# Kernel optimization log

Hardware: AMD Instinct MI355X
Metric: run time of the kernel (lower is better)

## Reference

```python
import jax, jax.numpy as jnp
import numpy as np

HID = 1024
NH = 16
HD = HID // NH  # 64


def _lin_params(key, fan_in, fan_out):
    k1, k2 = jax.random.split(key)
    lim = 1.0 / np.sqrt(fan_in)
    W = jax.random.uniform(k1, (fan_in, fan_out), jnp.float32, -lim, lim)
    b = jax.random.uniform(k2, (fan_out,), jnp.float32, -lim, lim)
    return W, b


def setup_inputs() -> dict:
    key = jax.random.key(0)
    ks = jax.random.split(key, 12)
    B, S = 4, 1024
    inp = {
        'query': jax.random.normal(ks[0], (B, S, HID), jnp.float32),
        'key': jax.random.normal(ks[1], (B, S, HID), jnp.float32),
        'value': jax.random.normal(ks[2], (B, S, HID), jnp.float32),
    }
    inp['Wq'], inp['bq'] = _lin_params(ks[3], HID, HID)
    inp['Wk'], inp['bk'] = _lin_params(ks[4], HID, HID)
    inp['Wv'], inp['bv'] = _lin_params(ks[5], HID, HID)
    inp['Wp'], inp['bp'] = _lin_params(ks[6], HID, HID)
    inp['Wup'], inp['bup'] = _lin_params(ks[7], HD, 1)
    inp['Wud'], inp['bud'] = _lin_params(ks[8], HD, 1)
    inp['Wus'], inp['bus'] = _lin_params(ks[9], HID, NH)
    inp['Wo'], inp['bo'] = _lin_params(ks[10], HID, HID)
    return inp


def _split_heads(x, B, S):
    # [B,S,HID] -> [B,NH,S,HD]
    return x.reshape(B, S, NH, HD).transpose(0, 2, 1, 3)


def reference(query, key, value, Wq, bq, Wk, bk, Wv, bv, Wp, bp,
              Wup, bup, Wud, bud, Wus, bus, Wo, bo):
    B, S, _ = query.shape
    len_q = S

    q = query @ Wq + bq   # [B,S,HID]
    k = key @ Wk + bk
    v = value @ Wv + bv

    # Gaussian-window positional bias (per head, per query position)
    p = _split_heads(q @ Wp + bp, B, S)              # [B,NH,S,HD]
    tp = jnp.tanh(p)
    p_i = tp @ Wup + bup                             # [B,NH,S,1]
    z_i = tp @ Wud + bud                             # [B,NH,S,1]
    cen_pos = len_q * jax.nn.sigmoid(p_i)            # [B,NH,S,1]
    win_size = len_q * jax.nn.sigmoid(z_i)           # [B,NH,S,1]
    pos = jnp.arange(len_q, dtype=q.dtype)[None, None, None, :]  # [1,1,1,S]
    bias = (pos - cen_pos) ** 2 / (0.5 * win_size ** 2)          # [B,NH,S,S]

    # per-head alpha gate from raw query
    alpha = jax.nn.sigmoid(query @ Wus + bus)        # [B,S,NH]
    alpha = alpha.reshape(B, S, NH, 1).transpose(0, 2, 1, 3)  # [B,NH,S,1]

    qh = _split_heads(q, B, S)
    kh = _split_heads(k, B, S)
    vh = _split_heads(v, B, S)

    scale = 1.0 / jnp.sqrt(jnp.asarray(HD, q.dtype))
    scores = jnp.einsum('bhqd,bhkd->bhqk', qh, kh) * scale
    scores = scores - alpha * bias                   # inject gated Gaussian bias
    attn = jax.nn.softmax(scores, axis=-1)           # [B,NH,S,S]

    out = jnp.einsum('bhqk,bhkd->bhqd', attn, vh)    # [B,NH,S,HD]
    x = out.transpose(0, 2, 1, 3).reshape(B, S, HID)
    x = x @ Wo + bo
    return x, attn
```

## Files before the change

kernel.cpp:

```cpp
#include <hip/hip_runtime.h>
#include <hip/hip_bf16.h>
#include <math.h>

#define S_LEN 1024
#define HIDN  1024
#define NHEAD 16
#define HDIM  64
#define BATCH 4
#define MTOT  (BATCH * S_LEN)

typedef __attribute__((ext_vector_type(8))) short          bf16v8;
typedef __attribute__((ext_vector_type(8))) unsigned short u16v8;
typedef __attribute__((ext_vector_type(4))) unsigned short u16v4;
typedef __attribute__((ext_vector_type(4))) float          f32v4;

__device__ __forceinline__ unsigned short f2bf_rne(float x) {
    unsigned int u = __float_as_uint(x);
    unsigned int r = (u + 0x7fffu + ((u >> 16) & 1u)) >> 16;
    return (unsigned short)r;
}
__device__ __forceinline__ float bf2f(unsigned short h) {
    return __uint_as_float(((unsigned int)h) << 16);
}
__device__ __forceinline__ void split2(float x, unsigned short& h, unsigned short& l) {
    h = f2bf_rne(x);
    l = f2bf_rne(x - bf2f(h));
}

__global__ __launch_bounds__(256) void split_w4(
    const float* __restrict__ W0, const float* __restrict__ W1,
    const float* __restrict__ W2, const float* __restrict__ W3,
    unsigned short* __restrict__ Hbase, unsigned short* __restrict__ Lbase)
{
    __shared__ float T[64][65];
    const int t  = threadIdx.x;
    const int k0 = blockIdx.y * 64;
    const int n0 = blockIdx.x * 64;
    const int z  = blockIdx.z;
    const float* W = (z == 0) ? W0 : (z == 1) ? W1 : (z == 2) ? W2 : W3;
    unsigned short* H = Hbase + (size_t)z * 1024 * 1024;
    unsigned short* L = Lbase + (size_t)z * 1024 * 1024;

    const int r = t >> 4;
    const int c = (t & 15) * 4;
#pragma unroll
    for (int i = 0; i < 4; ++i) {
        const int rr = r + i * 16;
        const float4 v = *(const float4*)&W[(size_t)(k0 + rr) * 1024 + n0 + c];
        T[rr][c + 0] = v.x; T[rr][c + 1] = v.y;
        T[rr][c + 2] = v.z; T[rr][c + 3] = v.w;
    }
    __syncthreads();

    const int n  = t >> 2;
    const int ko = (t & 3) * 16;
    u16v8 h0, h1, l0, l1;
#pragma unroll
    for (int kk = 0; kk < 8; ++kk) {
        unsigned short hh, ll;
        split2(T[ko + kk][n], hh, ll);
        h0[kk] = hh; l0[kk] = ll;
    }
#pragma unroll
    for (int kk = 0; kk < 8; ++kk) {
        unsigned short hh, ll;
        split2(T[ko + 8 + kk][n], hh, ll);
        h1[kk] = hh; l1[kk] = ll;
    }
    unsigned short* Hp = &H[(size_t)(n0 + n) * 1024 + k0 + ko];
    unsigned short* Lp = &L[(size_t)(n0 + n) * 1024 + k0 + ko];
    *(u16v8*)(Hp)     = h0;
    *(u16v8*)(Hp + 8) = h1;
    *(u16v8*)(Lp)     = l0;
    *(u16v8*)(Lp + 8) = l1;
}

template<int AF32, int EPI>
__global__ __launch_bounds__(512, 2) void gemm_t(
    const float* __restrict__ Af,
    const unsigned short* __restrict__ Ah, const unsigned short* __restrict__ Al,
    const unsigned short* __restrict__ Bh, const unsigned short* __restrict__ Bl,
    const float* __restrict__ bias, float* __restrict__ Cf,
    unsigned short* __restrict__ Ch, unsigned short* __restrict__ Cl,
    const float* __restrict__ Wup, const float* __restrict__ Wud,
    const float* __restrict__ bup, const float* __restrict__ bud,
    const float* __restrict__ alpha, float* __restrict__ cenp,
    float* __restrict__ c0p)
{
    __shared__ short Ash[128][40];
    __shared__ short Asl[128][40];
    __shared__ short Bsh[64][40];
    __shared__ short Bsl[64][40];
    __shared__ float PSUP[2][128], PSUD[2][128];

    const int t    = threadIdx.x;
    const int bm   = blockIdx.y * 128;
    const int bn   = blockIdx.x * 64;
    const int lane = t & 63;
    const int wid  = t >> 6;
    const int wr   = wid >> 1;
    const int wc   = wid & 1;
    const int fr   = lane & 15;
    const int fq   = lane >> 4;
    const int ks   = fq * 8;

    f32v4 zero = {0.f, 0.f, 0.f, 0.f};
    f32v4 acc[2][2];
#pragma unroll
    for (int i = 0; i < 2; ++i)
#pragma unroll
        for (int j = 0; j < 2; ++j) acc[i][j] = zero;

    const int sra = t >> 2;
    const int sca = (t & 3) * 8;
    const int tb  = t & 255;
    const int srb = tb >> 2;
    const int scb = (tb & 3) * 8;
    const bool isBl = (t >= 256);
    const unsigned short* pB = isBl ? &Bl[(size_t)(bn + srb) * 1024 + scb]
                                    : &Bh[(size_t)(bn + srb) * 1024 + scb];
    const float* pAf = AF32 ? &Af[(size_t)(bm + sra) * 1024 + sca] : nullptr;
    const unsigned short* pAh = AF32 ? nullptr : &Ah[(size_t)(bm + sra) * 1024 + sca];
    const unsigned short* pAl = AF32 ? nullptr : &Al[(size_t)(bm + sra) * 1024 + sca];

    u16v8 rah, ral, rb;
    auto LOAD = [&](int k0) {
        if (AF32) {
            const float4 a0 = *(const float4*)(pAf + k0);
            const float4 a1 = *(const float4*)(pAf + k0 + 4);
            const float xs[8] = {a0.x, a0.y, a0.z, a0.w, a1.x, a1.y, a1.z, a1.w};
#pragma unroll
            for (int e = 0; e < 8; ++e) {
                unsigned short hh, ll;
                split2(xs[e], hh, ll);
                rah[e] = hh; ral[e] = ll;
            }
        } else {
            rah = *(const u16v8*)(pAh + k0);
            ral = *(const u16v8*)(pAl + k0);
        }
        rb = *(const u16v8*)(pB + k0);
    };

    LOAD(0);
    for (int k0 = 0; k0 < 1024; k0 += 32) {
        __syncthreads();
        *(u16v8*)&Ash[sra][sca] = rah;
        *(u16v8*)&Asl[sra][sca] = ral;
        if (isBl) *(u16v8*)&Bsl[srb][scb] = rb;
        else      *(u16v8*)&Bsh[srb][scb] = rb;
        __syncthreads();

        if (k0 + 32 < 1024) LOAD(k0 + 32);

        bf16v8 fah[2], fal[2], fbh[2], fbl[2];
#pragma unroll
        for (int i = 0; i < 2; ++i) {
            fah[i] = *(const bf16v8*)&Ash[wr * 32 + i * 16 + fr][ks];
            fal[i] = *(const bf16v8*)&Asl[wr * 32 + i * 16 + fr][ks];
        }
#pragma unroll
        for (int j = 0; j < 2; ++j) {
            fbh[j] = *(const bf16v8*)&Bsh[wc * 32 + j * 16 + fr][ks];
            fbl[j] = *(const bf16v8*)&Bsl[wc * 32 + j * 16 + fr][ks];
        }
#pragma unroll
        for (int i = 0; i < 2; ++i)
#pragma unroll
            for (int j = 0; j < 2; ++j) {
                acc[i][j] = __builtin_amdgcn_mfma_f32_16x16x32_bf16(
                    fah[i], fbh[j], acc[i][j], 0, 0, 0);
                acc[i][j] = __builtin_amdgcn_mfma_f32_16x16x32_bf16(
                    fah[i], fbl[j], acc[i][j], 0, 0, 0);
                acc[i][j] = __builtin_amdgcn_mfma_f32_16x16x32_bf16(
                    fal[i], fbh[j], acc[i][j], 0, 0, 0);
            }
    }

    if (EPI == 3) {
        float wupj[2], wudj[2];
        float bb[2];
#pragma unroll
        for (int j = 0; j < 2; ++j) {
            const int colL = wc * 32 + j * 16 + fr;
            wupj[j] = Wup[colL];
            wudj[j] = Wud[colL];
            bb[j]   = bias[bn + colL];
        }
        float su[2][4], sd[2][4];
#pragma unroll
        for (int i = 0; i < 2; ++i)
#pragma unroll
            for (int r = 0; r < 4; ++r) { su[i][r] = 0.f; sd[i][r] = 0.f; }
#pragma unroll
        for (int j = 0; j < 2; ++j)
#pragma unroll
            for (int i = 0; i < 2; ++i)
#pragma unroll
                for (int r = 0; r < 4; ++r) {
                    const float tv = tanhf(acc[i][j][r] + bb[j]);
                    su[i][r] = fmaf(tv, wupj[j], su[i][r]);
                    sd[i][r] = fmaf(tv, wudj[j], sd[i][r]);
                }
#pragma unroll
        for (int i = 0; i < 2; ++i)
#pragma unroll
            for (int r = 0; r < 4; ++r) {
                float a = su[i][r], d = sd[i][r];
                a += __shfl_xor(a, 1); d += __shfl_xor(d, 1);
                a += __shfl_xor(a, 2); d += __shfl_xor(d, 2);
                a += __shfl_xor(a, 4); d += __shfl_xor(d, 4);
                a += __shfl_xor(a, 8); d += __shfl_xor(d, 8);
                if (fr == 0) {
                    const int row = wr * 32 + i * 16 + fq * 4 + r;
                    PSUP[wc][row] = a;
                    PSUD[wc][row] = d;
                }
            }
        __syncthreads();
        if (t < 128) {
            const float ap = PSUP[0][t] + PSUP[1][t] + bup[0];
            const float az = PSUD[0][t] + PSUD[1][t] + bud[0];
            const float cenv = 1024.f / (1.f + expf(-ap));
            const float win  = 1024.f / (1.f + expf(-az));
            const int grow = bm + t;
            const int hd   = bn >> 6;
            const int zz   = (grow >> 10) * 16 + hd;
            const int s    = grow & 1023;
            const float al = alpha[(size_t)grow * 16 + hd];
            cenp[(size_t)zz * 1024 + s] = cenv;
            c0p[(size_t)zz * 1024 + s]  = al * 2.f / (win * win);
        }
        return;
    }

#pragma unroll
    for (int j = 0; j < 2; ++j) {
        const int col = bn + wc * 32 + j * 16 + fr;
        const float bb = bias[col];
#pragma unroll
        for (int i = 0; i < 2; ++i) {
            const int row0 = bm + wr * 32 + i * 16 + fq * 4;
            const f32v4 cv = acc[i][j];
            if (EPI == 2) {
                u16v4 h4, l4;
#pragma unroll
                for (int r = 0; r < 4; ++r) {
                    unsigned short hh, ll;
                    split2(cv[r] + bb, hh, ll);
                    h4[r] = hh; l4[r] = ll;
                }
                const size_t base =
                    ((size_t)((row0 >> 10) * 16 + (col >> 6)) * 64 + (col & 63)) * 1024
                    + (row0 & 1023);
                *(u16v4*)&Ch[base] = h4;
                *(u16v4*)&Cl[base] = l4;
            } else if (EPI == 1) {
#pragma unroll
                for (int r = 0; r < 4; ++r) {
                    unsigned short hh, ll;
                    split2(cv[r] + bb, hh, ll);
                    const size_t idx = (size_t)(row0 + r) * 1024 + col;
                    Ch[idx] = hh; Cl[idx] = ll;
                }
            } else {
#pragma unroll
                for (int r = 0; r < 4; ++r)
                    Cf[(size_t)(row0 + r) * 1024 + col] = cv[r] + bb;
            }
        }
    }
}

__global__ __launch_bounds__(256) void alpha_kernel(
    const float* __restrict__ X, const float* __restrict__ Wus,
    const float* __restrict__ bus, float* __restrict__ alpha)
{
    __shared__ float Ws[1024 * 16];
    const int t = threadIdx.x;
#pragma unroll
    for (int i = 0; i < 16; ++i) {
        const int idx = t + i * 256;
        *reinterpret_cast<float4*>(&Ws[idx * 4]) =
            *reinterpret_cast<const float4*>(&Wus[idx * 4]);
    }
    __syncthreads();

    const int r = t >> 4, c = t & 15;
    const size_t row = (size_t)blockIdx.x * 16 + r;
    const float* x = &X[row * 1024];
    float acc = 0.f;
    for (int kk = 0; kk < 1024; kk += 4) {
        const float4 xv = *reinterpret_cast<const float4*>(&x[kk]);
        acc = fmaf(xv.x, Ws[(kk + 0) * 16 + c], acc);
        acc = fmaf(xv.y, Ws[(kk + 1) * 16 + c], acc);
        acc = fmaf(xv.z, Ws[(kk + 2) * 16 + c], acc);
        acc = fmaf(xv.w, Ws[(kk + 3) * 16 + c], acc);
    }
    acc += bus[c];
    alpha[row * 16 + c] = 1.f / (1.f + expf(-acc));
}

#define M0_SHIFT 8.0f
__global__ __launch_bounds__(512, 2) void attn_fused(
    const unsigned short* __restrict__ qh, const unsigned short* __restrict__ ql,
    const unsigned short* __restrict__ kh, const unsigned short* __restrict__ kl,
    const unsigned short* __restrict__ vTh, const unsigned short* __restrict__ vTl,
    const float* __restrict__ cen, const float* __restrict__ c0,
    float* __restrict__ attn,
    unsigned short* __restrict__ oh, unsigned short* __restrict__ ol)
{
    __shared__ unsigned short KH[64][64], KL[64][64];
    __shared__ unsigned short VH[64][64], VL[64][64];
    __shared__ unsigned short PH[128][64], PL[128][64];
    __shared__ float CEN[128], C0S[128];
    __shared__ float LSUM[2][128];
    __shared__ float RINV[128];

    const int bid   = blockIdx.x;
    const int z     = ((bid >> 6) << 3) | (bid & 7);
    const int itile = (bid >> 3) & 7;
    const int i0    = itile * 128;
    const int bq    = z >> 4;
    const int hd    = z & 15;

    const int t    = threadIdx.x;
    const int lane = t & 63;
    const int wid  = t >> 6;
    const int wrp  = wid >> 1;
    const int wc   = wid & 1;
    const int fr   = lane & 15, fq = lane >> 4;

    if (t < 128) {
        CEN[t] = cen[(size_t)z * 1024 + i0 + t];
        C0S[t] = c0[(size_t)z * 1024 + i0 + t];
    }

    bf16v8 qfh_[2][2], qfl_[2][2];
#pragma unroll
    for (int i = 0; i < 2; ++i)
#pragma unroll
        for (int kk = 0; kk < 2; ++kk) {
            const size_t qa = (size_t)(bq * 1024 + i0 + wrp * 32 + i * 16 + fr) * 1024
                              + hd * 64 + kk * 32 + fq * 8;
            qfh_[i][kk] = *(const bf16v8*)&qh[qa];
            qfl_[i][kk] = *(const bf16v8*)&ql[qa];
        }

    float lsum[2][4];
#pragma unroll
    for (int i = 0; i < 2; ++i)
#pragma unroll
        for (int r = 0; r < 4; ++r) lsum[i][r] = 0.f;

    const f32v4 zero = {0.f, 0.f, 0.f, 0.f};

    const int srow = t >> 3;
    const int sseg = t & 7;
    const int ssl  = (sseg ^ (srow & 7)) * 8;
    const unsigned short* vhb = vTh + (size_t)z * 64 * 1024;
    const unsigned short* vlb = vTl + (size_t)z * 64 * 1024;

    u16v8 rkh, rkl, rvh, rvl;
    auto LOADK = [&](int j0) {
        const size_t ga = (size_t)(bq * 1024 + j0 + srow) * 1024 + hd * 64 + sseg * 8;
        rkh = *(const u16v8*)&kh[ga];
        rkl = *(const u16v8*)&kl[ga];
    };
    auto LOADV = [&](int j0) {
        const size_t va = (size_t)srow * 1024 + j0 + sseg * 8;
        rvh = *(const u16v8*)&vhb[va];
        rvl = *(const u16v8*)&vlb[va];
    };

    LOADK(0);
    for (int jt = 0; jt < 16; ++jt) {
        const int j0 = jt * 64;
        __syncthreads();
        *(u16v8*)&KH[srow][ssl] = rkh;
        *(u16v8*)&KL[srow][ssl] = rkl;
        __syncthreads();
        if (jt < 15) LOADK(j0 + 64);

        f32v4 acc[2][2];
#pragma unroll
        for (int i = 0; i < 2; ++i)
#pragma unroll
            for (int j2 = 0; j2 < 2; ++j2) acc[i][j2] = zero;

#pragma unroll
        for (int kk = 0; kk < 2; ++kk) {
            bf16v8 fbh[2], fbl[2];
#pragma unroll
            for (int j2 = 0; j2 < 2; ++j2) {
                const int rb = wc * 32 + j2 * 16 + fr;
                const int sb = ((kk * 4 + fq) ^ (rb & 7)) * 8;
                fbh[j2] = *(const bf16v8*)&KH[rb][sb];
                fbl[j2] = *(const bf16v8*)&KL[rb][sb];
            }
#pragma unroll
            for (int i = 0; i < 2; ++i)
#pragma unroll
                for (int j2 = 0; j2 < 2; ++j2) {
                    acc[i][j2] = __builtin_amdgcn_mfma_f32_16x16x32_bf16(
                        qfh_[i][kk], fbh[j2], acc[i][j2], 0, 0, 0);
                    acc[i][j2] = __builtin_amdgcn_mfma_f32_16x16x32_bf16(
                        qfh_[i][kk], fbl[j2], acc[i][j2], 0, 0, 0);
                    acc[i][j2] = __builtin_amdgcn_mfma_f32_16x16x32_bf16(
                        qfl_[i][kk], fbh[j2], acc[i][j2], 0, 0, 0);
                }
        }

#pragma unroll
        for (int i = 0; i < 2; ++i)
#pragma unroll
            for (int r = 0; r < 4; ++r) {
                const int row = wrp * 32 + i * 16 + fq * 4 + r;
                const float cv = CEN[row], cc = C0S[row];
                float al = 0.f;
#pragma unroll
                for (int j2 = 0; j2 < 2; ++j2) {
                    const int col = wc * 32 + j2 * 16 + fr;
                    const float dd = (float)(j0 + col) - cv;
                    const float s  = acc[i][j2][r] * 0.125f - cc * dd * dd;
                    al += __expf(s - M0_SHIFT);
                }
                lsum[i][r] += al;
            }
    }

#pragma unroll
    for (int i = 0; i < 2; ++i)
#pragma unroll
        for (int r = 0; r < 4; ++r) {
            float v = lsum[i][r];
            v += __shfl_xor(v, 1);
            v += __shfl_xor(v, 2);
            v += __shfl_xor(v, 4);
            v += __shfl_xor(v, 8);
            if (fr == 0) LSUM[wc][wrp * 32 + i * 16 + fq * 4 + r] = v;
        }
    __syncthreads();
    if (t < 128) RINV[t] = 1.f / (LSUM[0][t] + LSUM[1][t]);

    f32v4 acco[2][2];
#pragma unroll
    for (int i = 0; i < 2; ++i)
#pragma unroll
        for (int j = 0; j < 2; ++j) acco[i][j] = zero;

    float* attnZ = attn + (size_t)z * 1024 * 1024;

    LOADK(0);
    LOADV(0);
    for (int jt = 0; jt < 16; ++jt) {
        const int j0 = jt * 64;
        __syncthreads();
        *(u16v8*)&KH[srow][ssl] = rkh;
        *(u16v8*)&KL[srow][ssl] = rkl;
        *(u16v8*)&VH[srow][ssl] = rvh;
        *(u16v8*)&VL[srow][ssl] = rvl;
        __syncthreads();
        if (jt < 15) { LOADK(j0 + 64); LOADV(j0 + 64); }

        f32v4 acc[2][2];
#pragma unroll
        for (int i = 0; i < 2; ++i)
#pragma unroll
            for (int j2 = 0; j2 < 2; ++j2) acc[i][j2] = zero;

#pragma unroll
        for (int kk = 0; kk < 2; ++kk) {
            bf16v8 fbh[2], fbl[2];
#pragma unroll
            for (int j2 = 0; j2 < 2; ++j2) {
                const int rb = wc * 32 + j2 * 16 + fr;
                const int sb = ((kk * 4 + fq) ^ (rb & 7)) * 8;
                fbh[j2] = *(const bf16v8*)&KH[rb][sb];
                fbl[j2] = *(const bf16v8*)&KL[rb][sb];
            }
#pragma unroll
            for (int i = 0; i < 2; ++i)
#pragma unroll
                for (int j2 = 0; j2 < 2; ++j2) {
                    acc[i][j2] = __builtin_amdgcn_mfma_f32_16x16x32_bf16(
                        qfh_[i][kk], fbh[j2], acc[i][j2], 0, 0, 0);
                    acc[i][j2] = __builtin_amdgcn_mfma_f32_16x16x32_bf16(
                        qfh_[i][kk], fbl[j2], acc[i][j2], 0, 0, 0);
                    acc[i][j2] = __builtin_amdgcn_mfma_f32_16x16x32_bf16(
                        qfl_[i][kk], fbh[j2], acc[i][j2], 0, 0, 0);
                }
        }

#pragma unroll
        for (int i = 0; i < 2; ++i)
#pragma unroll
            for (int r = 0; r < 4; ++r) {
                const int row = wrp * 32 + i * 16 + fq * 4 + r;
                const float cv = CEN[row], cc = C0S[row], ri = RINV[row];
#pragma unroll
                for (int j2 = 0; j2 < 2; ++j2) {
                    const int col = wc * 32 + j2 * 16 + fr;
                    const float dd = (float)(j0 + col) - cv;
                    const float s  = acc[i][j2][r] * 0.125f - cc * dd * dd;
                    const float p  = __expf(s - M0_SHIFT) * ri;
                    attnZ[(size_t)(i0 + row) * 1024 + j0 + col] = p;
                    unsigned short hv, lv;
                    split2(p, hv, lv);
                    const int slot = ((col >> 3) ^ (row & 7)) * 8 + (col & 7);
                    PH[row][slot] = hv;
                    PL[row][slot] = lv;
                }
            }
        __syncthreads();

#pragma unroll
        for (int kk = 0; kk < 2; ++kk) {
            bf16v8 pah[2], pal[2], fbh[2], fbl[2];
#pragma unroll
            for (int iq = 0; iq < 2; ++iq) {
                const int rp = wrp * 32 + iq * 16 + fr;
                const int sp = ((kk * 4 + fq) ^ (rp & 7)) * 8;
                pah[iq] = *(const bf16v8*)&PH[rp][sp];
                pal[iq] = *(const bf16v8*)&PL[rp][sp];
            }
#pragma unroll
            for (int jd = 0; jd < 2; ++jd) {
                const int rb = wc * 32 + jd * 16 + fr;
                const int sb = ((kk * 4 + fq) ^ (rb & 7)) * 8;
                fbh[jd] = *(const bf16v8*)&VH[rb][sb];
                fbl[jd] = *(const bf16v8*)&VL[rb][sb];
            }
#pragma unroll
            for (int iq = 0; iq < 2; ++iq)
#pragma unroll
                for (int jd = 0; jd < 2; ++jd) {
                    acco[iq][jd] = __builtin_amdgcn_mfma_f32_16x16x32_bf16(
                        pah[iq], fbh[jd], acco[iq][jd], 0, 0, 0);
                    acco[iq][jd] = __builtin_amdgcn_mfma_f32_16x16x32_bf16(
                        pah[iq], fbl[jd], acco[iq][jd], 0, 0, 0);
                    acco[iq][jd] = __builtin_amdgcn_mfma_f32_16x16x32_bf16(
                        pal[iq], fbh[jd], acco[iq][jd], 0, 0, 0);
                }
        }
    }

#pragma unroll
    for (int jd = 0; jd < 2; ++jd) {
        const int dcol = wc * 32 + jd * 16 + fr;
#pragma unroll
        for (int iq = 0; iq < 2; ++iq) {
            const int row0 = i0 + wrp * 32 + iq * 16 + fq * 4;
            const f32v4 cv = acco[iq][jd];
#pragma unroll
            for (int r = 0; r < 4; ++r) {
                unsigned short hv, lv;
                split2(cv[r], hv, lv);
                const size_t idx = (size_t)(bq * 1024 + row0 + r) * 1024 + hd * 64 + dcol;
                oh[idx] = hv;
                ol[idx] = lv;
            }
        }
    }
}

extern "C" void kernel_launch(void* const* d_in, const int* in_sizes, int n_in,
                              void* d_out, int out_size, void* d_ws, size_t ws_size,
                              hipStream_t stream)
{
    const float* query = (const float*)d_in[0];
    const float* key_  = (const float*)d_in[1];
    const float* value = (const float*)d_in[2];
    const float* Wq  = (const float*)d_in[3];
    const float* bq  = (const float*)d_in[4];
    const float* Wk  = (const float*)d_in[5];
    const float* bk  = (const float*)d_in[6];
    const float* Wv  = (const float*)d_in[7];
    const float* bv  = (const float*)d_in[8];
    const float* Wp  = (const float*)d_in[9];
    const float* bp  = (const float*)d_in[10];
    const float* Wup = (const float*)d_in[11];
    const float* bup = (const float*)d_in[12];
    const float* Wud = (const float*)d_in[13];
    const float* bud = (const float*)d_in[14];
    const float* Wus = (const float*)d_in[15];
    const float* bus = (const float*)d_in[16];
    const float* Wo  = (const float*)d_in[17];
    const float* bo  = (const float*)d_in[18];

    float* x_out = (float*)d_out;
    float* attn  = x_out + (size_t)MTOT * HIDN;

    char* wsb = (char*)d_ws;
    unsigned short* qh  = (unsigned short*)(wsb);
    unsigned short* ql  = (unsigned short*)(wsb + (8u  << 20));
    unsigned short* kh  = (unsigned short*)(wsb + (16u << 20));
    unsigned short* kl  = (unsigned short*)(wsb + (24u << 20));
    unsigned short* vTh = (unsigned short*)(wsb + (32u << 20));
    unsigned short* vTl = (unsigned short*)(wsb + (40u << 20));
    unsigned short* oh  = (unsigned short*)(wsb + (48u << 20));
    unsigned short* ol  = (unsigned short*)(wsb + (56u << 20));
    float* alpha_ws = (float*)(wsb + (64u << 20));
    float* cen_ws   = (float*)(wsb + (64u << 20) + (256u << 10));
    float* c0_ws    = (float*)(wsb + (64u << 20) + (512u << 10));
    unsigned short* wh = (unsigned short*)attn;
    unsigned short* wl = wh + (size_t)4 * 1024 * 1024;
    unsigned short* w2h = qh;
    unsigned short* w2l = ql;

    const dim3 blk(256);
    const dim3 blk512(512);
    const dim3 ggemm(HIDN / 64, MTOT / 128);
    const size_t WSTEP = (size_t)1024 * 1024;

    split_w4<<<dim3(16, 16, 4), blk, 0, stream>>>(Wq, Wk, Wv, Wp, wh, wl);
    alpha_kernel<<<dim3(MTOT / 16), blk, 0, stream>>>(query, Wus, bus, alpha_ws);
    gemm_t<1, 1><<<ggemm, blk512, 0, stream>>>(
        query, nullptr, nullptr, wh, wl, bq, nullptr, qh, ql,
        nullptr, nullptr, nullptr, nullptr, nullptr, nullptr, nullptr);
    gemm_t<1, 1><<<ggemm, blk512, 0, stream>>>(
        key_, nullptr, nullptr, wh + WSTEP, wl + WSTEP, bk, nullptr, kh, kl,
        nullptr, nullptr, nullptr, nullptr, nullptr, nullptr, nullptr);
    gemm_t<1, 2><<<ggemm, blk512, 0, stream>>>(
        value, nullptr, nullptr, wh + 2 * WSTEP, wl + 2 * WSTEP, bv,
        nullptr, vTh, vTl,
        nullptr, nullptr, nullptr, nullptr, nullptr, nullptr, nullptr);
    gemm_t<0, 3><<<ggemm, blk512, 0, stream>>>(
        nullptr, qh, ql, wh + 3 * WSTEP, wl + 3 * WSTEP, bp, nullptr,
        nullptr, nullptr,
        Wup, Wud, bup, bud, alpha_ws, cen_ws, c0_ws);
    attn_fused<<<dim3(512), blk512, 0, stream>>>(
        qh, ql, kh, kl, vTh, vTl, cen_ws, c0_ws, attn, oh, ol);
    split_w4<<<dim3(16, 16, 1), blk, 0, stream>>>(Wo, Wo, Wo, Wo, w2h, w2l);
    gemm_t<0, 0><<<ggemm, blk512, 0, stream>>>(
        nullptr, oh, ol, w2h, w2l, bo, x_out, nullptr, nullptr,
        nullptr, nullptr, nullptr, nullptr, nullptr, nullptr, nullptr);
}
```

Measured before the change: 379.9 us.

## Fold Wq into Wp and batch Q/K/V/P projections into one GEMM launch

Precomputes the combined weight Wq·Wp and the combined bias bq·Wp+bp, so the positional projection reads the raw query directly instead of waiting on the Q projection. The four projections then run as a single batched grid launch (z dimension), removing serial dependencies and raising occupancy. The attention kernel also alternates K staging between two shared buffers to drop one barrier per tile, and wraps its MFMA loops with s_setprio. The extra weight-product GEMM adds work and changes rounding order of the p path.

```diff
diff --git a/kernel.cpp b/kernel.cpp
--- a/kernel.cpp
+++ b/kernel.cpp
@@ -75,23 +75,65 @@
     *(u16v8*)(Lp + 8) = l1;
 }
 
+__global__ __launch_bounds__(256) void bqp_kernel(
+    const float* __restrict__ bq, const float* __restrict__ Wp,
+    const float* __restrict__ bp, float* __restrict__ bqp)
+{
+    __shared__ float red[4][64];
+    const int t  = threadIdx.x;
+    const int n0 = blockIdx.x * 64;
+    const int nn = t & 63;
+    const int ch = t >> 6;
+    float s = 0.f;
+    for (int k = ch * 256; k < ch * 256 + 256; ++k)
+        s = fmaf(bq[k], Wp[(size_t)k * 1024 + n0 + nn], s);
+    red[ch][nn] = s;
+    __syncthreads();
+    if (t < 64)
+        bqp[n0 + nn] = red[0][nn] + red[1][nn] + red[2][nn] + red[3][nn] + bp[n0 + nn];
+}
+
+__global__ __launch_bounds__(256) void alpha_kernel(
+    const float* __restrict__ X, const float* __restrict__ Wus,
+    const float* __restrict__ bus, float* __restrict__ alpha)
+{
+    __shared__ float Ws[1024 * 16];
+    const int t = threadIdx.x;
+#pragma unroll
+    for (int i = 0; i < 16; ++i) {
+        const int idx = t + i * 256;
+        *reinterpret_cast<float4*>(&Ws[idx * 4]) =
+            *reinterpret_cast<const float4*>(&Wus[idx * 4]);
+    }
+    __syncthreads();
+
+    const int r = t >> 4, c = t & 15;
+    const size_t row = (size_t)blockIdx.x * 16 + r;
+    const float* x = &X[row * 1024];
+    float acc = 0.f;
+    for (int kk = 0; kk < 1024; kk += 4) {
+        const float4 xv = *reinterpret_cast<const float4*>(&x[kk]);
+        acc = fmaf(xv.x, Ws[(kk + 0) * 16 + c], acc);
+        acc = fmaf(xv.y, Ws[(kk + 1) * 16 + c], acc);
+        acc = fmaf(xv.z, Ws[(kk + 2) * 16 + c], acc);
+        acc = fmaf(xv.w, Ws[(kk + 3) * 16 + c], acc);
+    }
+    acc += bus[c];
+    alpha[row * 16 + c] = 1.f / (1.f + expf(-acc));
+}
+
 template<int AF32, int EPI>
 __global__ __launch_bounds__(512, 2) void gemm_t(
     const float* __restrict__ Af,
     const unsigned short* __restrict__ Ah, const unsigned short* __restrict__ Al,
     const unsigned short* __restrict__ Bh, const unsigned short* __restrict__ Bl,
     const float* __restrict__ bias, float* __restrict__ Cf,
-    unsigned short* __restrict__ Ch, unsigned short* __restrict__ Cl,
-    const float* __restrict__ Wup, const float* __restrict__ Wud,
-    const float* __restrict__ bup, const float* __restrict__ bud,
-    const float* __restrict__ alpha, float* __restrict__ cenp,
-    float* __restrict__ c0p)
+    unsigned short* __restrict__ Ch, unsigned short* __restrict__ Cl)
 {
     __shared__ short Ash[128][40];
     __shared__ short Asl[128][40];
     __shared__ short Bsh[64][40];
     __shared__ short Bsl[64][40];
-    __shared__ float PSUP[2][128], PSUD[2][128];
 
     const int t    = threadIdx.x;
     const int bm   = blockIdx.y * 128;
@@ -177,9 +219,140 @@
             }
     }
 
-    if (EPI == 3) {
-        float wupj[2], wudj[2];
-        float bb[2];
+#pragma unroll
+    for (int j = 0; j < 2; ++j) {
+        const int col = bn + wc * 32 + j * 16 + fr;
+        const float bb = (EPI == 4) ? 0.f : bias[col];
+#pragma unroll
+        for (int i = 0; i < 2; ++i) {
+            const int row0 = bm + wr * 32 + i * 16 + fq * 4;
+            const f32v4 cv = acc[i][j];
+            if (EPI == 4) {
+                u16v4 h4, l4;
+#pragma unroll
+                for (int r = 0; r < 4; ++r) {
+                    unsigned short hh, ll;
+                    split2(cv[r], hh, ll);
+                    h4[r] = hh; l4[r] = ll;
+                }
+                const size_t base = (size_t)col * 1024 + row0;
+                *(u16v4*)&Ch[base] = h4;
+                *(u16v4*)&Cl[base] = l4;
+            } else {
+#pragma unroll
+                for (int r = 0; r < 4; ++r)
+                    Cf[(size_t)(row0 + r) * 1024 + col] = cv[r] + bb;
+            }
+        }
+    }
+}
+
+__global__ __launch_bounds__(512, 2) void gemm_batched(
+    const float* __restrict__ query, const float* __restrict__ key_,
+    const float* __restrict__ value,
+    const unsigned short* __restrict__ wh, const unsigned short* __restrict__ wl,
+    const unsigned short* __restrict__ w5h, const unsigned short* __restrict__ w5l,
+    const float* __restrict__ bq, const float* __restrict__ bk,
+    const float* __restrict__ bv, const float* __restrict__ bqp,
+    unsigned short* __restrict__ qh, unsigned short* __restrict__ ql,
+    unsigned short* __restrict__ kh, unsigned short* __restrict__ kl,
+    unsigned short* __restrict__ vTh, unsigned short* __restrict__ vTl,
+    const float* __restrict__ Wup, const float* __restrict__ Wud,
+    const float* __restrict__ bup, const float* __restrict__ bud,
+    const float* __restrict__ alpha, float* __restrict__ cenp,
+    float* __restrict__ c0p)
+{
+    __shared__ short Ash[128][40];
+    __shared__ short Asl[128][40];
+    __shared__ short Bsh[64][40];
+    __shared__ short Bsl[64][40];
+    __shared__ float PSUP[2][128], PSUD[2][128];
+
+    const int z    = blockIdx.z;
+    const float* Af = (z == 0 || z == 3) ? query : (z == 1) ? key_ : value;
+    const unsigned short* Bh = (z < 3) ? wh + (size_t)z * 1024 * 1024 : w5h;
+    const unsigned short* Bl = (z < 3) ? wl + (size_t)z * 1024 * 1024 : w5l;
+    const float* bias = (z == 0) ? bq : (z == 1) ? bk : (z == 2) ? bv : bqp;
+
+    const int t    = threadIdx.x;
+    const int bm   = blockIdx.y * 128;
+    const int bn   = blockIdx.x * 64;
+    const int lane = t & 63;
+    const int wid  = t >> 6;
+    const int wr   = wid >> 1;
+    const int wc   = wid & 1;
+    const int fr   = lane & 15;
+    const int fq   = lane >> 4;
+    const int ks   = fq * 8;
+
+    f32v4 zero = {0.f, 0.f, 0.f, 0.f};
+    f32v4 acc[2][2];
+#pragma unroll
+    for (int i = 0; i < 2; ++i)
+#pragma unroll
+        for (int j = 0; j < 2; ++j) acc[i][j] = zero;
+
+    const int sra = t >> 2;
+    const int sca = (t & 3) * 8;
+    const int tb  = t & 255;
+    const int srb = tb >> 2;
+    const int scb = (tb & 3) * 8;
+    const bool isBl = (t >= 256);
+    const unsigned short* pB = isBl ? &Bl[(size_t)(bn + srb) * 1024 + scb]
+                                    : &Bh[(size_t)(bn + srb) * 1024 + scb];
+    const float* pAf = &Af[(size_t)(bm + sra) * 1024 + sca];
+
+    u16v8 rah, ral, rb;
+    auto LOAD = [&](int k0) {
+        const float4 a0 = *(const float4*)(pAf + k0);
+        const float4 a1 = *(const float4*)(pAf + k0 + 4);
+        const float xs[8] = {a0.x, a0.y, a0.z, a0.w, a1.x, a1.y, a1.z, a1.w};
+#pragma unroll
+        for (int e = 0; e < 8; ++e) {
+            unsigned short hh, ll;
+            split2(xs[e], hh, ll);
+            rah[e] = hh; ral[e] = ll;
+        }
+        rb = *(const u16v8*)(pB + k0);
+    };
+
+    LOAD(0);
+    for (int k0 = 0; k0 < 1024; k0 += 32) {
+        __syncthreads();
+        *(u16v8*)&Ash[sra][sca] = rah;
+        *(u16v8*)&Asl[sra][sca] = ral;
+        if (isBl) *(u16v8*)&Bsl[srb][scb] = rb;
+        else      *(u16v8*)&Bsh[srb][scb] = rb;
+        __syncthreads();
+
+        if (k0 + 32 < 1024) LOAD(k0 + 32);
+
+        bf16v8 fah[2], fal[2], fbh[2], fbl[2];
+#pragma unroll
+        for (int i = 0; i < 2; ++i) {
+            fah[i] = *(const bf16v8*)&Ash[wr * 32 + i * 16 + fr][ks];
+            fal[i] = *(const bf16v8*)&Asl[wr * 32 + i * 16 + fr][ks];
+        }
+#pragma unroll
+        for (int j = 0; j < 2; ++j) {
+            fbh[j] = *(const bf16v8*)&Bsh[wc * 32 + j * 16 + fr][ks];
+            fbl[j] = *(const bf16v8*)&Bsl[wc * 32 + j * 16 + fr][ks];
+        }
+#pragma unroll
+        for (int i = 0; i < 2; ++i)
+#pragma unroll
+            for (int j = 0; j < 2; ++j) {
+                acc[i][j] = __builtin_amdgcn_mfma_f32_16x16x32_bf16(
+                    fah[i], fbh[j], acc[i][j], 0, 0, 0);
+                acc[i][j] = __builtin_amdgcn_mfma_f32_16x16x32_bf16(
+                    fah[i], fbl[j], acc[i][j], 0, 0, 0);
+                acc[i][j] = __builtin_amdgcn_mfma_f32_16x16x32_bf16(
+                    fal[i], fbh[j], acc[i][j], 0, 0, 0);
+            }
+    }
+
+    if (z == 3) {
+        float wupj[2], wudj[2], bb[2];
 #pragma unroll
         for (int j = 0; j < 2; ++j) {
             const int colL = wc * 32 + j * 16 + fr;
@@ -234,6 +407,9 @@
         return;
     }
 
+    unsigned short* Ch = (z == 0) ? qh : (z == 1) ? kh : vTh;
+    unsigned short* Cl = (z == 0) ? ql : (z == 1) ? kl : vTl;
+
 #pragma unroll
     for (int j = 0; j < 2; ++j) {
         const int col = bn + wc * 32 + j * 16 + fr;
@@ -242,7 +418,7 @@
         for (int i = 0; i < 2; ++i) {
             const int row0 = bm + wr * 32 + i * 16 + fq * 4;
             const f32v4 cv = acc[i][j];
-            if (EPI == 2) {
+            if (z == 2) {
                 u16v4 h4, l4;
 #pragma unroll
                 for (int r = 0; r < 4; ++r) {
@@ -255,7 +431,7 @@
                     + (row0 & 1023);
                 *(u16v4*)&Ch[base] = h4;
                 *(u16v4*)&Cl[base] = l4;
-            } else if (EPI == 1) {
+            } else {
 #pragma unroll
                 for (int r = 0; r < 4; ++r) {
                     unsigned short hh, ll;
@@ -263,42 +439,9 @@
                     const size_t idx = (size_t)(row0 + r) * 1024 + col;
                     Ch[idx] = hh; Cl[idx] = ll;
                 }
-            } else {
-#pragma unroll
-                for (int r = 0; r < 4; ++r)
-                    Cf[(size_t)(row0 + r) * 1024 + col] = cv[r] + bb;
-            }
-        }
-    }
-}
-
-__global__ __launch_bounds__(256) void alpha_kernel(
-    const float* __restrict__ X, const float* __restrict__ Wus,
-    const float* __restrict__ bus, float* __restrict__ alpha)
-{
-    __shared__ float Ws[1024 * 16];
-    const int t = threadIdx.x;
-#pragma unroll
-    for (int i = 0; i < 16; ++i) {
-        const int idx = t + i * 256;
-        *reinterpret_cast<float4*>(&Ws[idx * 4]) =
-            *reinterpret_cast<const float4*>(&Wus[idx * 4]);
-    }
-    __syncthreads();
-
-    const int r = t >> 4, c = t & 15;
-    const size_t row = (size_t)blockIdx.x * 16 + r;
-    const float* x = &X[row * 1024];
-    float acc = 0.f;
-    for (int kk = 0; kk < 1024; kk += 4) {
-        const float4 xv = *reinterpret_cast<const float4*>(&x[kk]);
-        acc = fmaf(xv.x, Ws[(kk + 0) * 16 + c], acc);
-        acc = fmaf(xv.y, Ws[(kk + 1) * 16 + c], acc);
-        acc = fmaf(xv.z, Ws[(kk + 2) * 16 + c], acc);
-        acc = fmaf(xv.w, Ws[(kk + 3) * 16 + c], acc);
-    }
-    acc += bus[c];
-    alpha[row * 16 + c] = 1.f / (1.f + expf(-acc));
+            }
+        }
+    }
 }
 
 #define M0_SHIFT 8.0f
@@ -376,9 +519,10 @@
     LOADK(0);
     for (int jt = 0; jt < 16; ++jt) {
         const int j0 = jt * 64;
-        __syncthreads();
-        *(u16v8*)&KH[srow][ssl] = rkh;
-        *(u16v8*)&KL[srow][ssl] = rkl;
+        unsigned short (*KHc)[64] = (jt & 1) ? VH : KH;
+        unsigned short (*KLc)[64] = (jt & 1) ? VL : KL;
+        *(u16v8*)&KHc[srow][ssl] = rkh;
+        *(u16v8*)&KLc[srow][ssl] = rkl;
         __syncthreads();
         if (jt < 15) LOADK(j0 + 64);
 
@@ -388,6 +532,7 @@
 #pragma unroll
             for (int j2 = 0; j2 < 2; ++j2) acc[i][j2] = zero;
 
+        __builtin_amdgcn_s_setprio(1);
 #pragma unroll
         for (int kk = 0; kk < 2; ++kk) {
             bf16v8 fbh[2], fbl[2];
@@ -395,8 +540,8 @@
             for (int j2 = 0; j2 < 2; ++j2) {
                 const int rb = wc * 32 + j2 * 16 + fr;
                 const int sb = ((kk * 4 + fq) ^ (rb & 7)) * 8;
-                fbh[j2] = *(const bf16v8*)&KH[rb][sb];
-                fbl[j2] = *(const bf16v8*)&KL[rb][sb];
+                fbh[j2] = *(const bf16v8*)&KHc[rb][sb];
+                fbl[j2] = *(const bf16v8*)&KLc[rb][sb];
             }
 #pragma unroll
             for (int i = 0; i < 2; ++i)
@@ -410,6 +555,7 @@
                         qfl_[i][kk], fbh[j2], acc[i][j2], 0, 0, 0);
                 }
         }
+        __builtin_amdgcn_s_setprio(0);
 
 #pragma unroll
         for (int i = 0; i < 2; ++i)
@@ -469,6 +615,7 @@
 #pragma unroll
             for (int j2 = 0; j2 < 2; ++j2) acc[i][j2] = zero;
 
+        __builtin_amdgcn_s_setprio(1);
 #pragma unroll
         for (int kk = 0; kk < 2; ++kk) {
             bf16v8 fbh[2], fbl[2];
@@ -491,6 +638,7 @@
                         qfl_[i][kk], fbh[j2], acc[i][j2], 0, 0, 0);
                 }
         }
+        __builtin_amdgcn_s_setprio(0);
 
 #pragma unroll
         for (int i = 0; i < 2; ++i)
@@ -514,6 +662,7 @@
             }
         __syncthreads();
 
+        __builtin_amdgcn_s_setprio(1);
 #pragma unroll
         for (int kk = 0; kk < 2; ++kk) {
             bf16v8 pah[2], pal[2], fbh[2], fbl[2];
@@ -543,6 +692,7 @@
                         pal[iq], fbh[jd], acco[iq][jd], 0, 0, 0);
                 }
         }
+        __builtin_amdgcn_s_setprio(0);
     }
 
 #pragma unroll
@@ -603,36 +753,33 @@
     float* alpha_ws = (float*)(wsb + (64u << 20));
     float* cen_ws   = (float*)(wsb + (64u << 20) + (256u << 10));
     float* c0_ws    = (float*)(wsb + (64u << 20) + (512u << 10));
-    unsigned short* wh = (unsigned short*)attn;
-    unsigned short* wl = wh + (size_t)4 * 1024 * 1024;
+    float* bqp_ws   = (float*)(wsb + (64u << 20) + (768u << 10));
+    unsigned short* wh  = (unsigned short*)attn;
+    unsigned short* wl  = wh + (size_t)4 * 1024 * 1024;
+    unsigned short* w5h = wl + (size_t)4 * 1024 * 1024;
+    unsigned short* w5l = w5h + (size_t)1024 * 1024;
     unsigned short* w2h = qh;
     unsigned short* w2l = ql;
 
     const dim3 blk(256);
     const dim3 blk512(512);
-    const dim3 ggemm(HIDN / 64, MTOT / 128);
     const size_t WSTEP = (size_t)1024 * 1024;
-
+    (void)WSTEP;
+
+    bqp_kernel<<<dim3(16), blk, 0, stream>>>(bq, Wp, bp, bqp_ws);
     split_w4<<<dim3(16, 16, 4), blk, 0, stream>>>(Wq, Wk, Wv, Wp, wh, wl);
     alpha_kernel<<<dim3(MTOT / 16), blk, 0, stream>>>(query, Wus, bus, alpha_ws);
-    gemm_t<1, 1><<<ggemm, blk512, 0, stream>>>(
-        query, nullptr, nullptr, wh, wl, bq, nullptr, qh, ql,
-        nullptr, nullptr, nullptr, nullptr, nullptr, nullptr, nullptr);
-    gemm_t<1, 1><<<ggemm, blk512, 0, stream>>>(
-        key_, nullptr, nullptr, wh + WSTEP, wl + WSTEP, bk, nullptr, kh, kl,
-        nullptr, nullptr, nullptr, nullptr, nullptr, nullptr, nullptr);
-    gemm_t<1, 2><<<ggemm, blk512, 0, stream>>>(
-        value, nullptr, nullptr, wh + 2 * WSTEP, wl + 2 * WSTEP, bv,
-        nullptr, vTh, vTl,
-        nullptr, nullptr, nullptr, nullptr, nullptr, nullptr, nullptr);
-    gemm_t<0, 3><<<ggemm, blk512, 0, stream>>>(
-        nullptr, qh, ql, wh + 3 * WSTEP, wl + 3 * WSTEP, bp, nullptr,
-        nullptr, nullptr,
+    gemm_t<1, 4><<<dim3(16, 8), blk512, 0, stream>>>(
+        Wq, nullptr, nullptr, wh + 3 * WSTEP, wl + 3 * WSTEP,
+        nullptr, nullptr, w5h, w5l);
+    gemm_batched<<<dim3(16, 32, 4), blk512, 0, stream>>>(
+        query, key_, value, wh, wl, w5h, w5l,
+        bq, bk, bv, bqp_ws,
+        qh, ql, kh, kl, vTh, vTl,
         Wup, Wud, bup, bud, alpha_ws, cen_ws, c0_ws);
     attn_fused<<<dim3(512), blk512, 0, stream>>>(
         qh, ql, kh, kl, vTh, vTl, cen_ws, c0_ws, attn, oh, ol);
     split_w4<<<dim3(16, 16, 1), blk, 0, stream>>>(Wo, Wo, Wo, Wo, w2h, w2l);
-    gemm_t<0, 0><<<ggemm, blk512, 0, stream>>>(
-        nullptr, oh, ol, w2h, w2l, bo, x_out, nullptr, nullptr,
-        nullptr, nullptr, nullptr, nullptr, nullptr, nullptr, nullptr);
-}
+    gemm_t<0, 0><<<dim3(16, 32), blk512, 0, stream>>>(
+        nullptr, oh, ol, w2h, w2l, bo, x_out, nullptr, nullptr);
+}
```

Result: slower. 394.8 us (+3.9%).
